# Kernel tuning notes

Measured on AMD Instinct MI355X. Metric: run time of the kernel, lower is better.

Reference implementation:

```python
import jax, jax.numpy as jnp
import numpy as np

NUM_HEADS = 8
HEAD_DIM = 64
D_MODEL = NUM_HEADS * HEAD_DIM  # 512
B, T = 4, 2048


def setup_inputs() -> dict:
    key = jax.random.key(0)
    k1, k2 = jax.random.split(key)
    x = jax.random.normal(k1, (B, T, D_MODEL), dtype=jnp.float32)
    mask = jnp.ones((B, 1, T, T), dtype=jnp.float32)
    W = jax.random.normal(k2, (D_MODEL, 3 * D_MODEL), dtype=jnp.float32) * (D_MODEL ** -0.5)
    b = jnp.zeros((3 * D_MODEL,), dtype=jnp.float32)
    return {"x": x, "mask": mask, "W": W, "b": b}


def reference(x, mask, W, b):
    batch = x.shape[0]
    # fused QKV projection: [B, T, 3D]
    qkv = jnp.einsum("btd,de->bte", x, W) + b
    # NOTE: faithful to torch reshape [B, T, H, Hd, 3] -> the size-3 axis is innermost
    qkv = qkv.reshape(batch, -1, NUM_HEADS, HEAD_DIM, 3)
    qkv = jnp.transpose(qkv, (4, 0, 2, 1, 3))  # [3, B, H, T, Hd]
    q, k, v = qkv[0], qkv[1], qkv[2]
    logits = jnp.einsum("bhqd,bhkd->bhqk", q, k) / (HEAD_DIM ** 0.5)
    logits = logits + (1.0 - mask) * -10000.0
    w = jax.nn.softmax(logits, axis=-1)
    out = jnp.einsum("bhqk,bhkd->bhqd", w, v)  # [B, H, T, Hd]
    out = jnp.transpose(out, (0, 2, 1, 3)).reshape(batch, -1, NUM_HEADS * HEAD_DIM)
    return out
```

## Files before the change

### kernel.cpp

```cpp
#include <hip/hip_runtime.h>
#include <hip/hip_bf16.h>
#include <stdint.h>

#define B_   4
#define T_   2048
#define H_   8
#define HD_  64
#define DM_  512
#define N3_  1536

typedef short bf_el;
typedef __attribute__((ext_vector_type(8))) bf_el bfrag;
typedef __attribute__((ext_vector_type(4))) bf_el bhalf4;
typedef __attribute__((ext_vector_type(4))) float ffrag;

#define SCALE_L2E  0.18033688011112043f
#define MASK_L2E   14426.950408889634f

static __device__ __forceinline__ unsigned short f2bf(float f) {
    union { float f; unsigned int i; } v; v.f = f;
    unsigned int r = v.i + 0x7fff + ((v.i >> 16) & 1);
    return (unsigned short)(r >> 16);
}
static __device__ __forceinline__ unsigned short f2bf_fast(float f) {
    union { float f; unsigned int i; } v; v.f = f;
    return (unsigned short)((v.i + 0x8000u) >> 16);
}

static __device__ __forceinline__ unsigned int cvt_pk_bf16(float a, float b) {
    unsigned int r;
    asm("v_cvt_pk_bf16_f32 %0, %1, %2" : "=v"(r) : "v"(a), "v"(b));
    return r;
}

typedef __attribute__((address_space(1))) const unsigned int gu32;
typedef __attribute__((address_space(3))) unsigned int lu32;
static __device__ __forceinline__ void glds16(const unsigned short* g, unsigned short* l) {
    __builtin_amdgcn_global_load_lds((gu32*)g, (lu32*)l, 16, 0, 0);
}

#define VMCNT(n) do { asm volatile("s_waitcnt vmcnt(" #n ")" ::: "memory"); \
                      __builtin_amdgcn_sched_barrier(0); } while (0)

__global__ __launch_bounds__(256) void k_prep(const float* __restrict__ W,
                                              const float* __restrict__ X,
                                              const float* __restrict__ mask,
                                              unsigned short* __restrict__ Wt,
                                              unsigned short* __restrict__ Xb,
                                              int* __restrict__ flags) {
    __shared__ __align__(16) unsigned short Ls[64 * 72];
    const int bid = blockIdx.x;
    const int tid = threadIdx.x;

    if (bid < 512) {
        const int R0 = bid * 16;
        const int mb = R0 >> 11;
        const int q0 = R0 & 2047;
        const int e  = mb * 32 + (q0 >> 6);
        const int wave = tid >> 6, lane = tid & 63;
        unsigned int acc = 0u;
        const float* base = mask + (size_t)R0 * T_ + tid * 8;
#pragma unroll
        for (int rr = 0; rr < 16; ++rr) {
            const uint4 u0 = *(const uint4*)(base + (size_t)rr * T_);
            const uint4 u1 = *(const uint4*)(base + (size_t)rr * T_ + 4);
            acc |= (u0.x ^ 0x3F800000u) | (u0.y ^ 0x3F800000u) |
                   (u0.z ^ 0x3F800000u) | (u0.w ^ 0x3F800000u) |
                   (u1.x ^ 0x3F800000u) | (u1.y ^ 0x3F800000u) |
                   (u1.z ^ 0x3F800000u) | (u1.w ^ 0x3F800000u);
        }
        unsigned long long bal = __ballot(acc != 0u);
        if (lane == 0) {
            unsigned int byte = 0u;
#pragma unroll
            for (int j = 0; j < 8; ++j)
                if ((bal >> (8 * j)) & 0xFFULL) byte |= (1u << j);
            ((unsigned char*)flags)[((size_t)e * 4 + (bid & 3)) * 4 + wave] =
                (unsigned char)byte;
        }
        return;
    }
    if (bid < 768) {
        const int b2 = bid - 512;
        const float* src = X + (size_t)b2 * 16384;
        unsigned short* dst = Xb + (size_t)b2 * 16384;
#pragma unroll
        for (int j = 0; j < 8; ++j) {
            int idx = j * 512 + tid * 2;
            float4 f0 = *(const float4*)(src + idx * 4);
            float4 f1 = *(const float4*)(src + idx * 4 + 4);
            __align__(16) unsigned short t8[8];
            t8[0] = f2bf_fast(f0.x); t8[1] = f2bf_fast(f0.y);
            t8[2] = f2bf_fast(f0.z); t8[3] = f2bf_fast(f0.w);
            t8[4] = f2bf_fast(f1.x); t8[5] = f2bf_fast(f1.y);
            t8[6] = f2bf_fast(f1.z); t8[7] = f2bf_fast(f1.w);
            *(uint4*)(dst + idx * 4) = *(const uint4*)t8;
        }
        return;
    }
    {
        const int t  = bid - 768;
        const int n0 = (t % 24) * 64;
        const int k0 = (t / 24) * 64;
#pragma unroll
        for (int i = 0; i < 4; ++i) {
            int chunk = tid + i * 256;
            int k = chunk >> 4;
            int c = chunk & 15;
            float4 f = *(const float4*)(W + (size_t)(k0 + k) * N3_ + n0 + c * 4);
            unsigned short* p = Ls + k * 72 + c * 4;
            p[0] = f2bf(f.x); p[1] = f2bf(f.y); p[2] = f2bf(f.z); p[3] = f2bf(f.w);
        }
        __syncthreads();
        const int n = tid >> 2;
        const int g = tid & 3;
        __align__(16) unsigned short tmp[16];
#pragma unroll
        for (int i = 0; i < 16; ++i) tmp[i] = Ls[(g * 16 + i) * 72 + n];
        uint4* dst = (uint4*)(Wt + (size_t)(n0 + n) * DM_ + k0 + g * 16);
        dst[0] = *(const uint4*)(tmp);
        dst[1] = *(const uint4*)(tmp + 8);
    }
}

__global__ __launch_bounds__(256) void k_gemm_qkv(const unsigned short* __restrict__ Xb,
                                                  const unsigned short* __restrict__ Wt,
                                                  const float* __restrict__ bias,
                                                  unsigned short* __restrict__ Qb,
                                                  unsigned short* __restrict__ Kb,
                                                  unsigned short* __restrict__ Vtb) {
    __shared__ __align__(16) unsigned short SH[40960];
    unsigned short* Cs = SH;

    const int tid  = threadIdx.x;
    const int wave = tid >> 6;
    const int lane = tid & 63;
    const int quad = lane >> 4;
    const int l16  = lane & 15;
    const int wm = wave >> 1, wn = wave & 1;
    const int h  = blockIdx.x >> 6;
    const int m0 = (blockIdx.x & 63) * 128;
    const int n0 = h * 192;

    float bvv[6];
#pragma unroll
    for (int ni = 0; ni < 6; ++ni) bvv[ni] = bias[n0 + wn * 96 + ni * 16 + l16];

    ffrag acc[4][6];
#pragma unroll
    for (int i = 0; i < 4; ++i)
#pragma unroll
        for (int j = 0; j < 6; ++j) acc[i][j] = (ffrag){0.f, 0.f, 0.f, 0.f};

    const int lrow = lane >> 2;
    const int gslot = (lane & 3) ^ (lrow & 3);
    const unsigned short* Ag = Xb + (size_t)(m0 + wave * 32 + lrow) * DM_ + gslot * 8;
    const unsigned short* Bg = Wt + (size_t)(n0 + wave * 48 + lrow) * DM_ + gslot * 8;

    auto STAGE = [&](int buf, int kt) {
        unsigned short* AL = SH + buf * 10240 + wave * 1024;
        unsigned short* BL = SH + buf * 10240 + 4096 + wave * 1536;
        const unsigned short* ag = Ag + kt * 32;
        const unsigned short* bg = Bg + kt * 32;
        glds16(ag, AL);
        glds16(ag + (size_t)16 * DM_, AL + 512);
        glds16(bg, BL);
        glds16(bg + (size_t)16 * DM_, BL + 512);
        glds16(bg + (size_t)32 * DM_, BL + 1024);
    };

    STAGE(0, 0);
    STAGE(1, 1);

    for (int kt = 0; kt < 16; ++kt) {
        if (kt < 14) STAGE((kt + 2) & 3, kt + 2);
        if (kt < 14)      { VMCNT(10); }
        else if (kt == 14){ VMCNT(5); }
        else              { VMCNT(0); }
        __builtin_amdgcn_s_barrier();

        const unsigned short* As = SH + (kt & 3) * 10240;
        const unsigned short* Bs = As + 4096;
        const int rslot = (quad ^ (l16 & 3)) * 8;
        bfrag af[4], bfr[6];
#pragma unroll
        for (int mi = 0; mi < 4; ++mi)
            af[mi] = *(const bfrag*)(As + (wm * 64 + mi * 16 + l16) * 32 + rslot);
#pragma unroll
        for (int ni = 0; ni < 6; ++ni)
            bfr[ni] = *(const bfrag*)(Bs + (wn * 96 + ni * 16 + l16) * 32 + rslot);
        __builtin_amdgcn_s_setprio(1);
#pragma unroll
        for (int mi = 0; mi < 4; ++mi)
#pragma unroll
            for (int ni = 0; ni < 6; ++ni)
                acc[mi][ni] = __builtin_amdgcn_mfma_f32_16x16x32_bf16(af[mi], bfr[ni], acc[mi][ni], 0, 0, 0);
        __builtin_amdgcn_s_setprio(0);
    }

    const int b   = m0 >> 11;
    const int tb0 = m0 & 2047;
    const size_t bh = (size_t)(b * 8 + h);
    float cscale[6];
#pragma unroll
    for (int ni = 0; ni < 6; ++ni) {
        int c = wn * 96 + ni * 16 + l16;
        cscale[ni] = (c % 3 == 0) ? SCALE_L2E : 1.0f;
    }
#pragma unroll
    for (int half = 0; half < 2; ++half) {
        __syncthreads();
        if (wm == half) {
#pragma unroll
            for (int mi = 0; mi < 4; ++mi)
#pragma unroll
                for (int ni = 0; ni < 6; ++ni)
#pragma unroll
                    for (int reg = 0; reg < 4; ++reg) {
                        int r = mi * 16 + quad * 4 + reg;
                        int c = wn * 96 + ni * 16 + l16;
                        Cs[r * 200 + c] = f2bf_fast((acc[mi][ni][reg] + bvv[ni]) * cscale[ni]);
                    }
        }
        __syncthreads();
        const int tb = tb0 + half * 64;
#pragma unroll
        for (int i = 0; i < 2; ++i) {
            int idx = tid + i * 256;
            int tl = idx >> 3, hc = (idx & 7) * 8;
            __align__(16) unsigned short tq[8], tk[8];
#pragma unroll
            for (int j = 0; j < 8; ++j) {
                tq[j] = Cs[tl * 200 + (hc + j) * 3 + 0];
                tk[j] = Cs[tl * 200 + (hc + j) * 3 + 1];
            }
            *(uint4*)(Qb + (bh * T_ + tb + tl) * HD_ + hc) = *(const uint4*)tq;
            *(uint4*)(Kb + (bh * T_ + tb + tl) * HD_ + hc) = *(const uint4*)tk;
        }
#pragma unroll
        for (int i = 0; i < 2; ++i) {
            int idx = tid + i * 256;
            int hd = idx >> 3, t8 = (idx & 7) * 8;
            __align__(16) unsigned short tv[8];
#pragma unroll
            for (int j = 0; j < 8; ++j)
                tv[j] = Cs[(t8 + j) * 200 + hd * 3 + 2];
            *(uint4*)(Vtb + (bh * HD_ + hd) * T_ + tb + t8) = *(const uint4*)tv;
        }
    }
}

__global__ __launch_bounds__(256, 2) void k_attn(const unsigned short* __restrict__ Q,
                                                 const unsigned short* __restrict__ K,
                                                 const unsigned short* __restrict__ Vt,
                                                 const float* __restrict__ mask,
                                                 const int* __restrict__ flags,
                                                 float* __restrict__ out) {
    __shared__ __align__(16) unsigned short SH[32768];
    __shared__ float Rs[256];

    const int tid = threadIdx.x;
    const int wave = tid >> 6, lane = tid & 63;
    const int quad = lane >> 4, l16 = lane & 15;
    const int rg = wave & 1;
    const int kh = wave >> 1;
    const int bh = blockIdx.x & 31, b = bh >> 3, h = bh & 7;
    const int qt = blockIdx.x >> 5;
    const int q0 = qt * 128;

    bfrag qf[4][2];
#pragma unroll
    for (int g = 0; g < 4; ++g) {
        size_t qrow = ((size_t)bh * T_ + q0 + rg * 64 + g * 16 + l16) * HD_;
        qf[g][0] = *(const bfrag*)(Q + qrow + quad * 8);
        qf[g][1] = *(const bfrag*)(Q + qrow + 32 + quad * 8);
    }
    ffrag of[4][5];
#pragma unroll
    for (int g = 0; g < 4; ++g)
#pragma unroll
        for (int nb = 0; nb < 5; ++nb) of[g][nb] = (ffrag){0.f, 0.f, 0.f, 0.f};

    bfrag vones;
#pragma unroll
    for (int j = 0; j < 8; ++j) vones[j] = (short)0x3F80;

    const int e = b * 32 + qt * 2 + rg;
    const int4 fw = *(const int4*)(flags + (size_t)e * 4);
    const unsigned int flbits = (unsigned int)(fw.x | fw.y | fw.z | fw.w);

    const int lrow = lane >> 3, lcol = lane & 7, swz = lcol ^ lrow;
    const int voffK = lrow * 64 + swz * 8;
    const size_t voffV = (size_t)(wave * 16 + lrow) * T_ + swz * 8;
    const unsigned short* Kbh = K  + (size_t)bh * T_ * HD_;
    const unsigned short* Vbh = Vt + (size_t)bh * HD_ * T_;

    auto STAGE = [&](int buf, int kt) {
        unsigned short* KL = &SH[buf * 4096] + wave * 1024;
        unsigned short* VL = &SH[16384 + buf * 4096] + wave * 1024;
        const unsigned short* kg = Kbh + (size_t)kt * 4096 + wave * 1024 + voffK;
        const unsigned short* vg = Vbh + (size_t)kt * 64 + voffV;
        glds16(kg, KL);
        glds16(kg + 512, KL + 512);
        glds16(vg, VL);
        glds16(vg + (size_t)8 * T_, VL + 512);
    };

    STAGE(0, 0);
    STAGE(1, 1);

    for (int kt = 0; kt < 32; ++kt) {
        if (kt < 30) STAGE((kt + 2) & 3, kt + 2);
        if (kt < 30)      { VMCNT(8); }
        else if (kt == 30){ VMCNT(4); }
        else              { VMCNT(0); }
        __builtin_amdgcn_s_barrier();

        const int cur = kt & 3;
        const unsigned short* KLc = &SH[cur * 4096];
        const unsigned short* VLc = &SH[16384 + cur * 4096];

        bfrag kf[2][2];
#pragma unroll
        for (int ns = 0; ns < 2; ++ns) {
            const int r = (kh * 2 + ns) * 16 + l16;
#pragma unroll
            for (int ks = 0; ks < 2; ++ks)
                kf[ns][ks] = *(const bfrag*)(KLc + r * 64 + (((ks * 4 + quad) ^ (l16 & 7)) * 8));
        }
        bhalf4 vf[2][4];
#pragma unroll
        for (int nb = 0; nb < 4; ++nb) {
            const int d = nb * 16 + l16;
#pragma unroll
            for (int ns = 0; ns < 2; ++ns)
                vf[ns][nb] = *(const bhalf4*)(VLc + d * 64 +
                                ((kh * 32 + ns * 16 + quad * 4) ^ ((l16 & 7) * 8)));
        }

        const int fl = (int)((flbits >> kt) & 1u);
#pragma unroll
        for (int g = 0; g < 4; ++g) {
            ffrag st[2];
            __builtin_amdgcn_s_setprio(1);
#pragma unroll
            for (int ns = 0; ns < 2; ++ns) {
                ffrag a = (ffrag){0.f, 0.f, 0.f, 0.f};
                a = __builtin_amdgcn_mfma_f32_16x16x32_bf16(kf[ns][0], qf[g][0], a, 0, 0, 0);
                a = __builtin_amdgcn_mfma_f32_16x16x32_bf16(kf[ns][1], qf[g][1], a, 0, 0, 0);
                st[ns] = a;
            }
            __builtin_amdgcn_s_setprio(0);
            float p[2][4];
            if (fl) {
                const float* mrow = mask + ((size_t)b * T_ + q0 + rg * 64 + g * 16 + l16) * T_
                                  + kt * 64 + kh * 32 + quad * 4;
#pragma unroll
                for (int ns = 0; ns < 2; ++ns) {
                    float mv[4];
                    *(float4*)mv = *(const float4*)(mrow + ns * 16);
#pragma unroll
                    for (int reg = 0; reg < 4; ++reg)
                        p[ns][reg] = __builtin_amdgcn_exp2f(
                            fmaf(mv[reg], MASK_L2E, st[ns][reg] - MASK_L2E));
                }
            } else {
#pragma unroll
                for (int ns = 0; ns < 2; ++ns)
#pragma unroll
                    for (int reg = 0; reg < 4; ++reg)
                        p[ns][reg] = __builtin_amdgcn_exp2f(st[ns][reg]);
            }
            union { unsigned int u[4]; bfrag s; } pa;
            pa.u[0] = cvt_pk_bf16(p[0][0], p[0][1]);
            pa.u[1] = cvt_pk_bf16(p[0][2], p[0][3]);
            pa.u[2] = cvt_pk_bf16(p[1][0], p[1][1]);
            pa.u[3] = cvt_pk_bf16(p[1][2], p[1][3]);
            __builtin_amdgcn_s_setprio(1);
#pragma unroll
            for (int nb = 0; nb < 4; ++nb) {
                union { bhalf4 h[2]; bfrag f; } vv;
                vv.h[0] = vf[0][nb];
                vv.h[1] = vf[1][nb];
                of[g][nb] = __builtin_amdgcn_mfma_f32_16x16x32_bf16(pa.s, vv.f, of[g][nb], 0, 0, 0);
            }
            of[g][4] = __builtin_amdgcn_mfma_f32_16x16x32_bf16(pa.s, vones, of[g][4], 0, 0, 0);
            __builtin_amdgcn_s_setprio(0);
        }
    }

    __syncthreads();
    float* Fp = (float*)SH;
    if (l16 == 0) {
#pragma unroll
        for (int g = 0; g < 4; ++g)
#pragma unroll
            for (int reg = 0; reg < 4; ++reg)
                Rs[kh * 128 + rg * 64 + g * 16 + quad * 4 + reg] = of[g][4][reg];
    }
    if (kh == 1) {
        float* basep = Fp + rg * (64 * 66);
#pragma unroll
        for (int g = 0; g < 4; ++g)
#pragma unroll
            for (int nb = 0; nb < 4; ++nb)
#pragma unroll
                for (int reg = 0; reg < 4; ++reg)
                    basep[(g * 16 + quad * 4 + reg) * 66 + nb * 16 + l16] = of[g][nb][reg];
    }
    __syncthreads();
    if (kh == 0) {
        const float* basep = Fp + rg * (64 * 66);
#pragma unroll
        for (int g = 0; g < 4; ++g) {
            float inv[4];
#pragma unroll
            for (int reg = 0; reg < 4; ++reg) {
                int row = rg * 64 + g * 16 + quad * 4 + reg;
                inv[reg] = 1.0f / (Rs[row] + Rs[128 + row]);
            }
#pragma unroll
            for (int nb = 0; nb < 4; ++nb)
#pragma unroll
                for (int reg = 0; reg < 4; ++reg) {
                    float v = of[g][nb][reg] + basep[(g * 16 + quad * 4 + reg) * 66 + nb * 16 + l16];
                    int t = q0 + rg * 64 + g * 16 + quad * 4 + reg;
                    out[((size_t)b * T_ + t) * DM_ + h * 64 + nb * 16 + l16] = v * inv[reg];
                }
        }
    }
}

extern "C" void kernel_launch(void* const* d_in, const int* in_sizes, int n_in,
                              void* d_out, int out_size, void* d_ws, size_t ws_size,
                              hipStream_t stream) {
    const float* X    = (const float*)d_in[0];
    const float* mask = (const float*)d_in[1];
    const float* W    = (const float*)d_in[2];
    const float* bias = (const float*)d_in[3];
    float* outp = (float*)d_out;

    char* ws = (char*)d_ws;
    unsigned short* Wt  = (unsigned short*)(ws);
    unsigned short* Xb  = (unsigned short*)(ws + 1572864);
    unsigned short* Qb  = (unsigned short*)(ws + 9961472);
    unsigned short* Kb  = (unsigned short*)(ws + 18350080);
    unsigned short* Vtb = (unsigned short*)(ws + 26738688);
    int*            flg = (int*)(ws + 35127296);

    k_prep     <<<dim3(960), 256, 0, stream>>>(W, X, mask, Wt, Xb, flg);
    k_gemm_qkv <<<dim3(512), 256, 0, stream>>>(Xb, Wt, bias, Qb, Kb, Vtb);
    k_attn     <<<dim3(512), 256, 0, stream>>>(Qb, Kb, Vtb, mask, flg, outp);
}
```

Baseline: 183.5 us.

## Move mask scan from prep kernel into QKV GEMM kernel as interleaved blocks

The mask-flag scan blocks move out of k_prep and into k_gemm_qkv, whose grid is doubled and split into GEMM and mask-scan roles in groups of 16 blocks. The bandwidth-heavy 64 MB mask read is meant to overlap with the compute-bound GEMM instead of sitting on the critical path of the prep kernel. The GEMM blocks keep their large LDS allocation, which may limit how many mask-scan blocks can be co-resident, and the two roles now compete for CU slots.

Result: slower. 197.5 us (+7.6%).

```diff
diff --git a/kernel.cpp b/kernel.cpp
--- a/kernel.cpp
+++ b/kernel.cpp
@@ -44,46 +44,15 @@
 
 __global__ __launch_bounds__(256) void k_prep(const float* __restrict__ W,
                                               const float* __restrict__ X,
-                                              const float* __restrict__ mask,
                                               unsigned short* __restrict__ Wt,
-                                              unsigned short* __restrict__ Xb,
-                                              int* __restrict__ flags) {
+                                              unsigned short* __restrict__ Xb) {
     __shared__ __align__(16) unsigned short Ls[64 * 72];
     const int bid = blockIdx.x;
     const int tid = threadIdx.x;
 
-    if (bid < 512) {
-        const int R0 = bid * 16;
-        const int mb = R0 >> 11;
-        const int q0 = R0 & 2047;
-        const int e  = mb * 32 + (q0 >> 6);
-        const int wave = tid >> 6, lane = tid & 63;
-        unsigned int acc = 0u;
-        const float* base = mask + (size_t)R0 * T_ + tid * 8;
-#pragma unroll
-        for (int rr = 0; rr < 16; ++rr) {
-            const uint4 u0 = *(const uint4*)(base + (size_t)rr * T_);
-            const uint4 u1 = *(const uint4*)(base + (size_t)rr * T_ + 4);
-            acc |= (u0.x ^ 0x3F800000u) | (u0.y ^ 0x3F800000u) |
-                   (u0.z ^ 0x3F800000u) | (u0.w ^ 0x3F800000u) |
-                   (u1.x ^ 0x3F800000u) | (u1.y ^ 0x3F800000u) |
-                   (u1.z ^ 0x3F800000u) | (u1.w ^ 0x3F800000u);
-        }
-        unsigned long long bal = __ballot(acc != 0u);
-        if (lane == 0) {
-            unsigned int byte = 0u;
-#pragma unroll
-            for (int j = 0; j < 8; ++j)
-                if ((bal >> (8 * j)) & 0xFFULL) byte |= (1u << j);
-            ((unsigned char*)flags)[((size_t)e * 4 + (bid & 3)) * 4 + wave] =
-                (unsigned char)byte;
-        }
-        return;
-    }
-    if (bid < 768) {
-        const int b2 = bid - 512;
-        const float* src = X + (size_t)b2 * 16384;
-        unsigned short* dst = Xb + (size_t)b2 * 16384;
+    if (bid < 256) {
+        const float* src = X + (size_t)bid * 16384;
+        unsigned short* dst = Xb + (size_t)bid * 16384;
 #pragma unroll
         for (int j = 0; j < 8; ++j) {
             int idx = j * 512 + tid * 2;
@@ -99,7 +68,7 @@
         return;
     }
     {
-        const int t  = bid - 768;
+        const int t  = bid - 256;
         const int n0 = (t % 24) * 64;
         const int k0 = (t / 24) * 64;
 #pragma unroll
@@ -128,18 +97,53 @@
                                                   const float* __restrict__ bias,
                                                   unsigned short* __restrict__ Qb,
                                                   unsigned short* __restrict__ Kb,
-                                                  unsigned short* __restrict__ Vtb) {
+                                                  unsigned short* __restrict__ Vtb,
+                                                  const float* __restrict__ mask,
+                                                  int* __restrict__ flags) {
     __shared__ __align__(16) unsigned short SH[40960];
     unsigned short* Cs = SH;
 
+    const int bid  = blockIdx.x;
     const int tid  = threadIdx.x;
+    const int role = (bid >> 4) & 1;
+    const int sub  = ((bid >> 5) << 4) | (bid & 15);
+
+    if (role) {
+        const int R0 = sub * 16;
+        const int mb = R0 >> 11;
+        const int q0m = R0 & 2047;
+        const int e  = mb * 32 + (q0m >> 6);
+        const int wv = tid >> 6, lane = tid & 63;
+        unsigned int acc = 0u;
+        const float* base = mask + (size_t)R0 * T_ + tid * 8;
+#pragma unroll
+        for (int rr = 0; rr < 16; ++rr) {
+            const uint4 u0 = *(const uint4*)(base + (size_t)rr * T_);
+            const uint4 u1 = *(const uint4*)(base + (size_t)rr * T_ + 4);
+            acc |= (u0.x ^ 0x3F800000u) | (u0.y ^ 0x3F800000u) |
+                   (u0.z ^ 0x3F800000u) | (u0.w ^ 0x3F800000u) |
+                   (u1.x ^ 0x3F800000u) | (u1.y ^ 0x3F800000u) |
+                   (u1.z ^ 0x3F800000u) | (u1.w ^ 0x3F800000u);
+        }
+        unsigned long long bal = __ballot(acc != 0u);
+        if (lane == 0) {
+            unsigned int byte = 0u;
+#pragma unroll
+            for (int j = 0; j < 8; ++j)
+                if ((bal >> (8 * j)) & 0xFFULL) byte |= (1u << j);
+            ((unsigned char*)flags)[((size_t)e * 4 + (sub & 3)) * 4 + wv] =
+                (unsigned char)byte;
+        }
+        return;
+    }
+
     const int wave = tid >> 6;
     const int lane = tid & 63;
     const int quad = lane >> 4;
     const int l16  = lane & 15;
     const int wm = wave >> 1, wn = wave & 1;
-    const int h  = blockIdx.x >> 6;
-    const int m0 = (blockIdx.x & 63) * 128;
+    const int h  = sub >> 6;
+    const int m0 = (sub & 63) * 128;
     const int n0 = h * 192;
 
     float bvv[6];
@@ -448,7 +452,7 @@
     unsigned short* Vtb = (unsigned short*)(ws + 26738688);
     int*            flg = (int*)(ws + 35127296);
 
-    k_prep     <<<dim3(960), 256, 0, stream>>>(W, X, mask, Wt, Xb, flg);
-    k_gemm_qkv <<<dim3(512), 256, 0, stream>>>(Xb, Wt, bias, Qb, Kb, Vtb);
-    k_attn     <<<dim3(512), 256, 0, stream>>>(Qb, Kb, Vtb, mask, flg, outp);
-}
+    k_prep     <<<dim3(448),  256, 0, stream>>>(W, X, Wt, Xb);
+    k_gemm_qkv <<<dim3(1024), 256, 0, stream>>>(Xb, Wt, bias, Qb, Kb, Vtb, mask, flg);
+    k_attn     <<<dim3(512),  256, 0, stream>>>(Qb, Kb, Vtb, mask, flg, outp);
+}
```
